# Optimization experiments

Measured on AMD Instinct MI355X. Metric: run time of the kernel, lower is better.

The kernel has to match this reference:

```python
import jax, jax.numpy as jnp
import numpy as np

NUM_NODES = 200000
NUM_EDGES = 1250000
DIM = 64
K_LAYERS = 3
BATCH = 4096
CAND = 101  # 1 positive + 100 negatives


def setup_inputs() -> dict:
    key = jax.random.key(0)
    k1, k2, k3 = jax.random.split(key, 3)
    emb = jax.random.normal(k1, (NUM_NODES, DIM), dtype=jnp.float32)
    edge_index = jax.random.randint(k2, (2, NUM_EDGES), 0, NUM_NODES)
    batch = jax.random.randint(k3, (BATCH, CAND, 3), 0, NUM_NODES)
    return {"emb": emb, "edge_index": edge_index, "batch": batch,
            "num_nodes": NUM_NODES}


def reference(emb, edge_index, batch, num_nodes):
    # --- LightGCN.get_embedding: K rounds of symmetric-normalized SpMM ---
    row, col = edge_index[0], edge_index[1]  # source -> target
    ones = jnp.ones(row.shape[0], dtype=emb.dtype)
    deg = jax.ops.segment_sum(ones, col, num_segments=num_nodes)  # in-degree
    deg_safe = jnp.where(deg > 0, deg, 1.0)
    dis = jnp.where(deg > 0, jax.lax.rsqrt(deg_safe), 0.0)  # deg^{-1/2}, inf->0
    norm = dis[row] * dis[col]  # [E]

    alpha = 1.0 / (K_LAYERS + 1)  # uniform layer combination
    x = emb
    out = x * alpha
    for _ in range(K_LAYERS):
        # propagate: out[i] = sum_{(j->i)} norm_e * x[j]
        x = jax.ops.segment_sum(x[row] * norm[:, None], col,
                                num_segments=num_nodes)
        out = out + x * alpha

    # --- scoring: gather user/item embeddings, elementwise dot ---
    user_idx = batch[:, :, 0].reshape(-1)
    item_idx = batch[:, :, 1].reshape(-1)
    logits = jnp.sum(out[user_idx] * out[item_idx], axis=-1)  # [B*CAND]
    return logits.reshape(batch.shape[0], -1)
```

## Files before the change

kernel.cpp:

```cpp
#include <hip/hip_runtime.h>

#define DIM 64
#define BSHIFT 8
#define MAXNB 1024
#define CHUNK 4096

__device__ inline unsigned packbf(float a, float b) {
    unsigned ua = __float_as_uint(a), ub = __float_as_uint(b);
    unsigned ra = (ua + 0x7FFFu + ((ua >> 16) & 1u)) >> 16;
    unsigned rb = (ub + 0x7FFFu + ((ub >> 16) & 1u)) >> 16;
    return ra | (rb << 16);
}
__device__ inline void unpackbf(unsigned u, float& lo, float& hi) {
    lo = __uint_as_float(u << 16);
    hi = __uint_as_float(u & 0xFFFF0000u);
}
__device__ inline void acc_row(const uint4 v, float* s) {
    float lo, hi;
    unpackbf(v.x, lo, hi); s[0] += lo; s[1] += hi;
    unpackbf(v.y, lo, hi); s[2] += lo; s[3] += hi;
    unpackbf(v.z, lo, hi); s[4] += lo; s[5] += hi;
    unpackbf(v.w, lo, hi); s[6] += lo; s[7] += hi;
}

__global__ void coarse_hist_kernel(const int* __restrict__ col,
                                   int* __restrict__ bcnt, int E, int NB) {
    __shared__ int h[MAXNB];
    for (int i = threadIdx.x; i < NB; i += 256) h[i] = 0;
    __syncthreads();
    int e = blockIdx.x * 256 + threadIdx.x;
    int stride = gridDim.x * 256;
    for (; e < E; e += stride) atomicAdd(&h[col[e] >> BSHIFT], 1);
    __syncthreads();
    for (int i = threadIdx.x; i < NB; i += 256) {
        int v = h[i];
        if (v) atomicAdd(&bcnt[i], v);
    }
}

__global__ void bucket_scan_kernel(const int* __restrict__ bcnt,
                                   int* __restrict__ bbase,
                                   int* __restrict__ bcursor, int NB, int E) {
    __shared__ int lds[256];
    int tid = threadIdx.x;
    int base = tid * 4;
    int c[4];
    int local = 0;
    #pragma unroll
    for (int k = 0; k < 4; k++) {
        c[k] = (base + k < NB) ? bcnt[base + k] : 0;
        local += c[k];
    }
    lds[tid] = local;
    __syncthreads();
    for (int off = 1; off < 256; off <<= 1) {
        int t = (tid >= off) ? lds[tid - off] : 0;
        __syncthreads();
        lds[tid] += t;
        __syncthreads();
    }
    int excl = lds[tid] - local;
    #pragma unroll
    for (int k = 0; k < 4; k++) {
        if (base + k < NB) {
            bbase[base + k] = excl;
            bcursor[base + k] = excl;
        }
        excl += c[k];
    }
    if (tid == 0) bbase[NB] = E;
}

__global__ __launch_bounds__(256) void scatter_binned_kernel(
        const int* __restrict__ row, const int* __restrict__ col,
        int* __restrict__ bcursor, unsigned* __restrict__ pairs, int E,
        int NB) {
    __shared__ unsigned stage[CHUNK];
    __shared__ int gdst[CHUNK];
    __shared__ int hist[MAXNB];
    __shared__ int pfx[MAXNB];
    __shared__ int gbase[MAXNB];
    int tid = threadIdx.x;
    int base = blockIdx.x * CHUNK;
    int nloc = min(CHUNK, E - base);

    for (int b = tid; b < NB; b += 256) hist[b] = 0;
    __syncthreads();

    unsigned vals[CHUNK / 256];
    int keys[CHUNK / 256];
    #pragma unroll
    for (int k = 0; k < CHUNK / 256; k++) {
        int e = base + tid + k * 256;
        if (e < E) {
            int d = col[e];
            int s = row[e];
            keys[k] = d >> BSHIFT;
            vals[k] = (unsigned)s | ((unsigned)(d & 255) << 24);
            atomicAdd(&hist[keys[k]], 1);
        } else {
            keys[k] = -1;
        }
    }
    __syncthreads();

    int b0 = tid * 4;
    int c4[4];
    int loc = 0;
    #pragma unroll
    for (int k = 0; k < 4; k++) {
        c4[k] = (b0 + k < NB) ? hist[b0 + k] : 0;
        loc += c4[k];
    }
    gbase[tid] = loc;
    __syncthreads();
    for (int off = 1; off < 256; off <<= 1) {
        int t = (tid >= off) ? gbase[tid - off] : 0;
        __syncthreads();
        gbase[tid] += t;
        __syncthreads();
    }
    int excl = gbase[tid] - loc;
    #pragma unroll
    for (int k = 0; k < 4; k++) {
        if (b0 + k < NB) pfx[b0 + k] = excl;
        excl += c4[k];
    }
    __syncthreads();

    for (int b = tid; b < NB; b += 256) {
        int c = hist[b];
        gbase[b] = (c > 0) ? atomicAdd(&bcursor[b], c) : 0;
        hist[b] = pfx[b];
    }
    __syncthreads();

    #pragma unroll
    for (int k = 0; k < CHUNK / 256; k++) {
        if (keys[k] >= 0) {
            int slot = atomicAdd(&hist[keys[k]], 1);
            stage[slot] = vals[k];
            gdst[slot] = gbase[keys[k]] + (slot - pfx[keys[k]]);
        }
    }
    __syncthreads();

    for (int s = tid; s < nloc; s += 256) pairs[gdst[s]] = stage[s];
}

__global__ void fine_fill_kernel(const unsigned* __restrict__ pairs,
                                 const int* __restrict__ bbase,
                                 int* __restrict__ row_ptr,
                                 int* __restrict__ csr_src, int N, int E) {
    __shared__ int cnt[256];
    __shared__ int cur[256];
    int b = blockIdx.x;
    int tid = threadIdx.x;
    int beg = bbase[b], end = bbase[b + 1];
    cnt[tid] = 0;
    __syncthreads();
    for (int j = beg + tid; j < end; j += 256)
        atomicAdd(&cnt[pairs[j] >> 24], 1);
    __syncthreads();
    int v = cnt[tid];
    for (int off = 1; off < 256; off <<= 1) {
        int t = (tid >= off) ? cnt[tid - off] : 0;
        __syncthreads();
        cnt[tid] += t;
        __syncthreads();
    }
    int excl = cnt[tid] - v;
    int node = (b << BSHIFT) + tid;
    if (node < N) row_ptr[node] = beg + excl;
    cur[tid] = beg + excl;
    __syncthreads();
    for (int j = beg + tid; j < end; j += 256) {
        unsigned p = pairs[j];
        int pos = atomicAdd(&cur[p >> 24], 1);
        csr_src[pos] = (int)(p & 0xFFFFFFu);
    }
    if (b == 0 && tid == 0) row_ptr[N] = E;
}

__global__ void prescale_kernel(const float4* __restrict__ emb4,
                                const int* __restrict__ row_ptr,
                                uint4* __restrict__ z4, int N) {
    int t = blockIdx.x * blockDim.x + threadIdx.x;
    int i = t >> 3;
    int gl = t & 7;
    if (i >= N) return;
    int deg = row_ptr[i + 1] - row_ptr[i];
    float wd = (deg > 0) ? rsqrtf((float)deg) : 0.0f;
    size_t eo = (size_t)i * 16 + gl * 2;
    float4 a = emb4[eo], b = emb4[eo + 1];
    uint4 z;
    z.x = packbf(a.x * wd, a.y * wd);
    z.y = packbf(a.z * wd, a.w * wd);
    z.z = packbf(b.x * wd, b.y * wd);
    z.w = packbf(b.z * wd, b.w * wd);
    z4[(size_t)i * 8 + gl] = z;
}

__global__ void spmm_pull_kernel(const int* __restrict__ row_ptr,
                                 const int* __restrict__ csr_src,
                                 const uint4* __restrict__ z4,
                                 uint4* __restrict__ znext4, int N) {
    int t = blockIdx.x * blockDim.x + threadIdx.x;
    int i = t >> 3;
    int gl = t & 7;
    if (i >= N) return;
    int b = row_ptr[i], e = row_ptr[i + 1];
    float s[8] = {0, 0, 0, 0, 0, 0, 0, 0};
    int j = b;
    for (; j + 3 < e; j += 4) {
        int i0 = csr_src[j], i1 = csr_src[j + 1];
        int i2 = csr_src[j + 2], i3 = csr_src[j + 3];
        uint4 v0 = z4[(size_t)i0 * 8 + gl];
        uint4 v1 = z4[(size_t)i1 * 8 + gl];
        uint4 v2 = z4[(size_t)i2 * 8 + gl];
        uint4 v3 = z4[(size_t)i3 * 8 + gl];
        acc_row(v0, s); acc_row(v1, s); acc_row(v2, s); acc_row(v3, s);
    }
    for (; j < e; ++j) {
        uint4 v = z4[(size_t)csr_src[j] * 8 + gl];
        acc_row(v, s);
    }
    int deg = e - b;
    float wd = (deg > 0) ? rsqrtf((float)deg) : 0.0f;
    float w2 = wd * wd;
    uint4 z;
    z.x = packbf(s[0] * w2, s[1] * w2);
    z.y = packbf(s[2] * w2, s[3] * w2);
    z.z = packbf(s[4] * w2, s[5] * w2);
    z.w = packbf(s[6] * w2, s[7] * w2);
    znext4[(size_t)i * 8 + gl] = z;
}

__global__ void spmm_combine_kernel(const int* __restrict__ row_ptr,
                                    const int* __restrict__ csr_src,
                                    const uint4* __restrict__ z2,
                                    const uint4* __restrict__ z1,
                                    const float4* __restrict__ emb4,
                                    uint4* __restrict__ accb, int N) {
    int t = blockIdx.x * blockDim.x + threadIdx.x;
    int i = t >> 3;
    int gl = t & 7;
    if (i >= N) return;
    int b = row_ptr[i], e = row_ptr[i + 1];
    float s[8] = {0, 0, 0, 0, 0, 0, 0, 0};
    int j = b;
    for (; j + 3 < e; j += 4) {
        int i0 = csr_src[j], i1 = csr_src[j + 1];
        int i2 = csr_src[j + 2], i3 = csr_src[j + 3];
        uint4 v0 = z2[(size_t)i0 * 8 + gl];
        uint4 v1 = z2[(size_t)i1 * 8 + gl];
        uint4 v2 = z2[(size_t)i2 * 8 + gl];
        uint4 v3 = z2[(size_t)i3 * 8 + gl];
        acc_row(v0, s); acc_row(v1, s); acc_row(v2, s); acc_row(v3, s);
    }
    for (; j < e; ++j) {
        uint4 v = z2[(size_t)csr_src[j] * 8 + gl];
        acc_row(v, s);
    }
    int deg = e - b;
    float wd = (deg > 0) ? rsqrtf((float)deg) : 0.0f;
    float sq = (deg > 0) ? sqrtf((float)deg) : 0.0f;
    size_t zo = (size_t)i * 8 + gl;
    uint4 a1 = z1[zo], a2 = z2[zo];
    float w[8] = {0, 0, 0, 0, 0, 0, 0, 0};
    acc_row(a1, w); acc_row(a2, w);
    size_t eo = (size_t)i * 16 + gl * 2;
    float4 e0 = emb4[eo], e1 = emb4[eo + 1];
    float r0 = e0.x + sq * w[0] + wd * s[0];
    float r1 = e0.y + sq * w[1] + wd * s[1];
    float r2 = e0.z + sq * w[2] + wd * s[2];
    float r3 = e0.w + sq * w[3] + wd * s[3];
    float r4 = e1.x + sq * w[4] + wd * s[4];
    float r5 = e1.y + sq * w[5] + wd * s[5];
    float r6 = e1.z + sq * w[6] + wd * s[6];
    float r7 = e1.w + sq * w[7] + wd * s[7];
    uint4 z;
    z.x = packbf(r0, r1);
    z.y = packbf(r2, r3);
    z.z = packbf(r4, r5);
    z.w = packbf(r6, r7);
    accb[zo] = z;
}

__global__ void score_kernel(const int* __restrict__ batch,
                             const uint4* __restrict__ accb,
                             float* __restrict__ out, int P) {
    int t = blockIdx.x * blockDim.x + threadIdx.x;
    int p = t >> 3;
    int gl = t & 7;
    if (p >= P) return;
    int u = batch[(size_t)p * 3 + 0];
    int it = batch[(size_t)p * 3 + 1];
    uint4 a = accb[(size_t)u * 8 + gl];
    uint4 b = accb[(size_t)it * 8 + gl];
    float sa[8] = {0, 0, 0, 0, 0, 0, 0, 0};
    float sb[8] = {0, 0, 0, 0, 0, 0, 0, 0};
    acc_row(a, sa);
    acc_row(b, sb);
    float s = sa[0] * sb[0] + sa[1] * sb[1] + sa[2] * sb[2] + sa[3] * sb[3] +
              sa[4] * sb[4] + sa[5] * sb[5] + sa[6] * sb[6] + sa[7] * sb[7];
    s += __shfl_xor(s, 4, 64);
    s += __shfl_xor(s, 2, 64);
    s += __shfl_xor(s, 1, 64);
    if (gl == 0) out[p] = s * 0.0625f;
}

extern "C" void kernel_launch(void* const* d_in, const int* in_sizes, int n_in,
                              void* d_out, int out_size, void* d_ws,
                              size_t ws_size, hipStream_t stream) {
    const float* emb = (const float*)d_in[0];
    const int* edge_index = (const int*)d_in[1];
    const int* batch = (const int*)d_in[2];
    float* out = (float*)d_out;

    const int N = in_sizes[0] / DIM;
    const int E = in_sizes[1] / 2;
    const int P = out_size;
    const int NB = (N + 255) >> BSHIFT;

    const int* row = edge_index;
    const int* col = edge_index + E;

    const size_t zbytes = (size_t)N * DIM * 2;

    auto align256 = [](size_t x) { return (x + 255) & ~(size_t)255; };
    char* ws = (char*)d_ws;
    uint4* z0   = (uint4*)ws; ws += align256(zbytes);
    uint4* z1   = (uint4*)ws; ws += align256(zbytes);
    uint4* z2   = (uint4*)ws; ws += align256(zbytes);
    uint4* accb = (uint4*)ws; ws += align256(zbytes);
    unsigned* pairs = (unsigned*)ws; ws += align256((size_t)E * 4);
    int* csr_src    = (int*)ws;      ws += align256((size_t)E * 4);
    int* row_ptr    = (int*)ws;      ws += align256((size_t)(N + 1) * 4);
    int* bcnt       = (int*)ws;      ws += align256((size_t)MAXNB * 4);
    int* bbase      = (int*)ws;      ws += align256((size_t)(MAXNB + 1) * 4);
    int* bcursor    = (int*)ws;

    hipMemsetAsync(bcnt, 0, (size_t)MAXNB * 4, stream);
    coarse_hist_kernel<<<1024, 256, 0, stream>>>(col, bcnt, E, NB);
    bucket_scan_kernel<<<1, 256, 0, stream>>>(bcnt, bbase, bcursor, NB, E);
    scatter_binned_kernel<<<(E + CHUNK - 1) / CHUNK, 256, 0, stream>>>(
        row, col, bcursor, pairs, E, NB);
    fine_fill_kernel<<<NB, 256, 0, stream>>>(pairs, bbase, row_ptr, csr_src,
                                             N, E);

    const int nodeBlocks = (N * 8 + 255) / 256;

    prescale_kernel<<<nodeBlocks, 256, 0, stream>>>((const float4*)emb,
                                                    row_ptr, z0, N);

    spmm_pull_kernel<<<nodeBlocks, 256, 0, stream>>>(row_ptr, csr_src, z0, z1, N);
    spmm_pull_kernel<<<nodeBlocks, 256, 0, stream>>>(row_ptr, csr_src, z1, z2, N);
    spmm_combine_kernel<<<nodeBlocks, 256, 0, stream>>>(row_ptr, csr_src, z2,
                                                        z1, (const float4*)emb,
                                                        accb, N);

    score_kernel<<<(P * 8 + 255) / 256, 256, 0, stream>>>(batch, accb, out, P);
}
```

Baseline: 271.3 us.

## Use per-block histogram scan for deterministic binning and prefetch CSR indices in gathers

Replaces the global-atomic coarse histogram plus per-block atomic cursor reservation with a per-block histogram matrix that is scanned bucket-major. Each scatter block then reads its precomputed output offsets directly, so edges are placed in a stable order. The SpMM gather loop is also rewritten to prefetch the next four column indices while the current rows load, and to mask the tail with multipliers instead of a scalar remainder loop. The binning change adds several small kernel launches and an M-sized scan in exchange for removing atomic contention.

```diff
diff --git a/kernel.cpp b/kernel.cpp
--- a/kernel.cpp
+++ b/kernel.cpp
@@ -22,35 +22,77 @@
     unpackbf(v.z, lo, hi); s[4] += lo; s[5] += hi;
     unpackbf(v.w, lo, hi); s[6] += lo; s[7] += hi;
 }
-
-__global__ void coarse_hist_kernel(const int* __restrict__ col,
-                                   int* __restrict__ bcnt, int E, int NB) {
+__device__ inline void acc_row_m(const uint4 v, float m, float* s) {
+    float lo, hi;
+    unpackbf(v.x, lo, hi); s[0] = fmaf(m, lo, s[0]); s[1] = fmaf(m, hi, s[1]);
+    unpackbf(v.y, lo, hi); s[2] = fmaf(m, lo, s[2]); s[3] = fmaf(m, hi, s[3]);
+    unpackbf(v.z, lo, hi); s[4] = fmaf(m, lo, s[4]); s[5] = fmaf(m, hi, s[5]);
+    unpackbf(v.w, lo, hi); s[6] = fmaf(m, lo, s[6]); s[7] = fmaf(m, hi, s[7]);
+}
+
+__global__ __launch_bounds__(256) void block_hist_kernel(
+        const int* __restrict__ col, int* __restrict__ H, int E, int NB,
+        int nblocks) {
     __shared__ int h[MAXNB];
-    for (int i = threadIdx.x; i < NB; i += 256) h[i] = 0;
-    __syncthreads();
-    int e = blockIdx.x * 256 + threadIdx.x;
-    int stride = gridDim.x * 256;
-    for (; e < E; e += stride) atomicAdd(&h[col[e] >> BSHIFT], 1);
-    __syncthreads();
-    for (int i = threadIdx.x; i < NB; i += 256) {
-        int v = h[i];
-        if (v) atomicAdd(&bcnt[i], v);
-    }
-}
-
-__global__ void bucket_scan_kernel(const int* __restrict__ bcnt,
-                                   int* __restrict__ bbase,
-                                   int* __restrict__ bcursor, int NB, int E) {
+    int tid = threadIdx.x;
+    for (int k = tid; k < NB; k += 256) h[k] = 0;
+    __syncthreads();
+    int base = blockIdx.x * CHUNK;
+    #pragma unroll
+    for (int k = 0; k < CHUNK / 256; k++) {
+        int e = base + tid + k * 256;
+        if (e < E) atomicAdd(&h[col[e] >> BSHIFT], 1);
+    }
+    __syncthreads();
+    for (int k = tid; k < NB; k += 256) H[(size_t)k * nblocks + blockIdx.x] = h[k];
+}
+
+__global__ void scan_tile_sum_kernel(const int* __restrict__ H,
+                                     int* __restrict__ T, int M) {
+    int tid = threadIdx.x;
+    int base = blockIdx.x * 1024 + tid * 4;
+    int s = 0;
+    #pragma unroll
+    for (int k = 0; k < 4; k++)
+        if (base + k < M) s += H[base + k];
     __shared__ int lds[256];
-    int tid = threadIdx.x;
-    int base = tid * 4;
+    lds[tid] = s;
+    __syncthreads();
+    for (int off = 128; off > 0; off >>= 1) {
+        if (tid < off) lds[tid] += lds[tid + off];
+        __syncthreads();
+    }
+    if (tid == 0) T[blockIdx.x] = lds[0];
+}
+
+__global__ void scan_tile_offsets_kernel(int* __restrict__ T, int nt) {
+    __shared__ int lds[256];
+    int tid = threadIdx.x;
+    int v = (tid < nt) ? T[tid] : 0;
+    lds[tid] = v;
+    __syncthreads();
+    for (int off = 1; off < 256; off <<= 1) {
+        int t = (tid >= off) ? lds[tid - off] : 0;
+        __syncthreads();
+        lds[tid] += t;
+        __syncthreads();
+    }
+    if (tid < nt) T[tid] = lds[tid] - v;
+}
+
+__global__ void scan_final_kernel(const int* __restrict__ H,
+                                  const int* __restrict__ T,
+                                  int* __restrict__ S, int M) {
+    int tid = threadIdx.x;
+    int base = blockIdx.x * 1024 + tid * 4;
     int c[4];
     int local = 0;
     #pragma unroll
     for (int k = 0; k < 4; k++) {
-        c[k] = (base + k < NB) ? bcnt[base + k] : 0;
+        c[k] = (base + k < M) ? H[base + k] : 0;
         local += c[k];
     }
+    __shared__ int lds[256];
     lds[tid] = local;
     __syncthreads();
     for (int off = 1; off < 256; off <<= 1) {
@@ -59,29 +101,33 @@
         lds[tid] += t;
         __syncthreads();
     }
-    int excl = lds[tid] - local;
+    int excl = lds[tid] - local + T[blockIdx.x];
     #pragma unroll
     for (int k = 0; k < 4; k++) {
-        if (base + k < NB) {
-            bbase[base + k] = excl;
-            bcursor[base + k] = excl;
-        }
+        if (base + k < M) S[base + k] = excl;
         excl += c[k];
     }
-    if (tid == 0) bbase[NB] = E;
+}
+
+__global__ void bbase_kernel(const int* __restrict__ S, int* __restrict__ bbase,
+                             int NB, int nblocks, int E) {
+    int k = blockIdx.x * blockDim.x + threadIdx.x;
+    if (k < NB) bbase[k] = S[(size_t)k * nblocks];
+    if (k == 0) bbase[NB] = E;
 }
 
 __global__ __launch_bounds__(256) void scatter_binned_kernel(
         const int* __restrict__ row, const int* __restrict__ col,
-        int* __restrict__ bcursor, unsigned* __restrict__ pairs, int E,
-        int NB) {
+        const int* __restrict__ S, unsigned* __restrict__ pairs, int E,
+        int NB, int nblocks) {
     __shared__ unsigned stage[CHUNK];
     __shared__ int gdst[CHUNK];
     __shared__ int hist[MAXNB];
     __shared__ int pfx[MAXNB];
     __shared__ int gbase[MAXNB];
     int tid = threadIdx.x;
-    int base = blockIdx.x * CHUNK;
+    int bid = blockIdx.x;
+    int base = bid * CHUNK;
     int nloc = min(CHUNK, E - base);
 
     for (int b = tid; b < NB; b += 256) hist[b] = 0;
@@ -129,8 +175,7 @@
     __syncthreads();
 
     for (int b = tid; b < NB; b += 256) {
-        int c = hist[b];
-        gbase[b] = (c > 0) ? atomicAdd(&bcursor[b], c) : 0;
+        gbase[b] = S[(size_t)b * nblocks + bid];
         hist[b] = pfx[b];
     }
     __syncthreads();
@@ -201,6 +246,39 @@
     z4[(size_t)i * 8 + gl] = z;
 }
 
+__device__ inline void row_gather_sum(const int* __restrict__ csr_src,
+                                      const uint4* __restrict__ z4, int b,
+                                      int e, int gl, float* s) {
+    if (b >= e) return;
+    int e1 = e - 1;
+    int j = b;
+    int i0 = csr_src[j];
+    int i1 = csr_src[min(j + 1, e1)];
+    int i2 = csr_src[min(j + 2, e1)];
+    int i3 = csr_src[min(j + 3, e1)];
+    while (j < e) {
+        uint4 v0 = z4[(size_t)i0 * 8 + gl];
+        uint4 v1 = z4[(size_t)i1 * 8 + gl];
+        uint4 v2 = z4[(size_t)i2 * 8 + gl];
+        uint4 v3 = z4[(size_t)i3 * 8 + gl];
+        int jn = j + 4;
+        if (jn < e) {
+            i0 = csr_src[jn];
+            i1 = csr_src[min(jn + 1, e1)];
+            i2 = csr_src[min(jn + 2, e1)];
+            i3 = csr_src[min(jn + 3, e1)];
+        }
+        float m1 = (j + 1 < e) ? 1.0f : 0.0f;
+        float m2 = (j + 2 < e) ? 1.0f : 0.0f;
+        float m3 = (j + 3 < e) ? 1.0f : 0.0f;
+        acc_row(v0, s);
+        acc_row_m(v1, m1, s);
+        acc_row_m(v2, m2, s);
+        acc_row_m(v3, m3, s);
+        j = jn;
+    }
+}
+
 __global__ void spmm_pull_kernel(const int* __restrict__ row_ptr,
                                  const int* __restrict__ csr_src,
                                  const uint4* __restrict__ z4,
@@ -211,20 +289,7 @@
     if (i >= N) return;
     int b = row_ptr[i], e = row_ptr[i + 1];
     float s[8] = {0, 0, 0, 0, 0, 0, 0, 0};
-    int j = b;
-    for (; j + 3 < e; j += 4) {
-        int i0 = csr_src[j], i1 = csr_src[j + 1];
-        int i2 = csr_src[j + 2], i3 = csr_src[j + 3];
-        uint4 v0 = z4[(size_t)i0 * 8 + gl];
-        uint4 v1 = z4[(size_t)i1 * 8 + gl];
-        uint4 v2 = z4[(size_t)i2 * 8 + gl];
-        uint4 v3 = z4[(size_t)i3 * 8 + gl];
-        acc_row(v0, s); acc_row(v1, s); acc_row(v2, s); acc_row(v3, s);
-    }
-    for (; j < e; ++j) {
-        uint4 v = z4[(size_t)csr_src[j] * 8 + gl];
-        acc_row(v, s);
-    }
+    row_gather_sum(csr_src, z4, b, e, gl, s);
     int deg = e - b;
     float wd = (deg > 0) ? rsqrtf((float)deg) : 0.0f;
     float w2 = wd * wd;
@@ -248,20 +313,7 @@
     if (i >= N) return;
     int b = row_ptr[i], e = row_ptr[i + 1];
     float s[8] = {0, 0, 0, 0, 0, 0, 0, 0};
-    int j = b;
-    for (; j + 3 < e; j += 4) {
-        int i0 = csr_src[j], i1 = csr_src[j + 1];
-        int i2 = csr_src[j + 2], i3 = csr_src[j + 3];
-        uint4 v0 = z2[(size_t)i0 * 8 + gl];
-        uint4 v1 = z2[(size_t)i1 * 8 + gl];
-        uint4 v2 = z2[(size_t)i2 * 8 + gl];
-        uint4 v3 = z2[(size_t)i3 * 8 + gl];
-        acc_row(v0, s); acc_row(v1, s); acc_row(v2, s); acc_row(v3, s);
-    }
-    for (; j < e; ++j) {
-        uint4 v = z2[(size_t)csr_src[j] * 8 + gl];
-        acc_row(v, s);
-    }
+    row_gather_sum(csr_src, z2, b, e, gl, s);
     int deg = e - b;
     float wd = (deg > 0) ? rsqrtf((float)deg) : 0.0f;
     float sq = (deg > 0) ? sqrtf((float)deg) : 0.0f;
@@ -322,6 +374,9 @@
     const int E = in_sizes[1] / 2;
     const int P = out_size;
     const int NB = (N + 255) >> BSHIFT;
+    const int nblocks = (E + CHUNK - 1) / CHUNK;
+    const int M = NB * nblocks;
+    const int nt = (M + 1023) / 1024;
 
     const int* row = edge_index;
     const int* col = edge_index + E;
@@ -337,15 +392,18 @@
     unsigned* pairs = (unsigned*)ws; ws += align256((size_t)E * 4);
     int* csr_src    = (int*)ws;      ws += align256((size_t)E * 4);
     int* row_ptr    = (int*)ws;      ws += align256((size_t)(N + 1) * 4);
-    int* bcnt       = (int*)ws;      ws += align256((size_t)MAXNB * 4);
-    int* bbase      = (int*)ws;      ws += align256((size_t)(MAXNB + 1) * 4);
-    int* bcursor    = (int*)ws;
-
-    hipMemsetAsync(bcnt, 0, (size_t)MAXNB * 4, stream);
-    coarse_hist_kernel<<<1024, 256, 0, stream>>>(col, bcnt, E, NB);
-    bucket_scan_kernel<<<1, 256, 0, stream>>>(bcnt, bbase, bcursor, NB, E);
-    scatter_binned_kernel<<<(E + CHUNK - 1) / CHUNK, 256, 0, stream>>>(
-        row, col, bcursor, pairs, E, NB);
+    int* H          = (int*)ws;      ws += align256((size_t)M * 4);
+    int* S          = (int*)ws;      ws += align256((size_t)M * 4);
+    int* T          = (int*)ws;      ws += align256(256 * 4);
+    int* bbase      = (int*)ws;
+
+    block_hist_kernel<<<nblocks, 256, 0, stream>>>(col, H, E, NB, nblocks);
+    scan_tile_sum_kernel<<<nt, 256, 0, stream>>>(H, T, M);
+    scan_tile_offsets_kernel<<<1, 256, 0, stream>>>(T, nt);
+    scan_final_kernel<<<nt, 256, 0, stream>>>(H, T, S, M);
+    bbase_kernel<<<(NB + 255) / 256, 256, 0, stream>>>(S, bbase, NB, nblocks, E);
+    scatter_binned_kernel<<<nblocks, 256, 0, stream>>>(row, col, S, pairs, E,
+                                                       NB, nblocks);
     fine_fill_kernel<<<NB, 256, 0, stream>>>(pairs, bbase, row_ptr, csr_src,
                                              N, E);
 
```

Measured after the change: 249.9 us. -7.9%, faster.
